# Optimization experiments

Hardware: AMD Instinct MI355X
Metric: run time of the kernel (lower is better)

## Reference

```python
import jax, jax.numpy as jnp
import numpy as np

HEADS = 16
NEG = -10000.0


def setup_inputs() -> dict:
    key = jax.random.key(0)
    ks = jax.random.split(key, 8)
    B, S, D = 2, 2048, 2048
    scale = 0.02
    return {
        "q": jax.random.normal(ks[0], (B, S, D), dtype=jnp.float32),
        "k": jax.random.normal(ks[1], (B, S, D), dtype=jnp.float32),
        "v": jax.random.normal(ks[2], (B, S, D), dtype=jnp.float32),
        "mask": jax.random.randint(ks[3], (B, S, S), 0, 2).astype(jnp.bool_),
        "Wq": jax.random.normal(ks[4], (D, D), dtype=jnp.float32) * scale,
        "Wk": jax.random.normal(ks[5], (D, D), dtype=jnp.float32) * scale,
        "Wv": jax.random.normal(ks[6], (D, D), dtype=jnp.float32) * scale,
        "Wo": jax.random.normal(ks[7], (D, D), dtype=jnp.float32) * scale,
    }


def _split_heads(x):
    # (B, S, D) -> (B, H, S, Dh)
    B, S, D = x.shape
    return x.reshape(B, S, HEADS, D // HEADS).transpose(0, 2, 1, 3)


def reference(q, k, v, mask, Wq, Wk, Wv, Wo):
    # bias-free linear projections (nn.Linear: x @ W.T)
    qp = q @ Wq.T
    kp = k @ Wk.T
    vp = v @ Wv.T
    qh, kh, vh = _split_heads(qp), _split_heads(kp), _split_heads(vp)
    head_dim = qh.shape[-1]
    # scores: (B, H, S, S)
    scores = jnp.einsum('bhqd,bhkd->bhqk', qh, kh) / jnp.sqrt(
        jnp.asarray(head_dim, dtype=qh.dtype))
    # additive mask, broadcast over heads (mask unsqueezed at -3 in torch)
    scores = scores + mask[:, None, :, :].astype(scores.dtype) * NEG
    attn = jax.nn.softmax(scores, axis=-1)
    ctx = jnp.einsum('bhqk,bhkd->bhqd', attn, vh)  # (B, H, S, Dh)
    B, H, S, Dh = ctx.shape
    ctx = ctx.transpose(0, 2, 1, 3).reshape(B, S, H * Dh)
    out = ctx @ Wo.T
    return (out, kp, vp)
```

## Files before the change

### kernel.cpp

```cpp
#include <hip/hip_runtime.h>
#include <hip/hip_bf16.h>
#include <stdint.h>


typedef unsigned short u16;
typedef unsigned char u8;
typedef __bf16 bf16x8 __attribute__((ext_vector_type(8)));
typedef unsigned short u16x8 __attribute__((ext_vector_type(8)));
typedef unsigned short u16x4 __attribute__((ext_vector_type(4)));
typedef float f32x4 __attribute__((ext_vector_type(4)));

#if __has_builtin(__builtin_amdgcn_exp2f)
#define EXP2(x) __builtin_amdgcn_exp2f(x)
#else
#define EXP2(x) exp2f(x)
#endif

__device__ __forceinline__ u16 f2bf(float f) {
  union { __bf16 h; u16 u; } c;
  c.h = (__bf16)f;
  return c.u;
}

__device__ __forceinline__ void stage8_f32(const float* src, u16* dst) {
  float4 x0 = ((const float4*)src)[0];
  float4 x1 = ((const float4*)src)[1];
  u16 t[8] = {f2bf(x0.x), f2bf(x0.y), f2bf(x0.z), f2bf(x0.w),
              f2bf(x1.x), f2bf(x1.y), f2bf(x1.z), f2bf(x1.w)};
  *(uint4*)dst = *(const uint4*)t;
}

typedef const __attribute__((address_space(1))) void gas_t;
typedef __attribute__((address_space(3))) void las_t;
__device__ __forceinline__ void gll16(const void* g, void* l) {
  __builtin_amdgcn_global_load_lds((gas_t*)g, (las_t*)l, 16, 0, 0);
}

__global__ void detect_kernel(const u16* __restrict__ q,
                              const u16* __restrict__ mask,
                              int* __restrict__ flags) {
  __shared__ int c32, oddnz, b3f80;
  if (threadIdx.x == 0) { c32 = 0; oddnz = 0; b3f80 = 0; }
  __syncthreads();
  int l32 = 0, lodd = 0, l3f = 0;
  for (int i = threadIdx.x; i < 4096; i += 256) {
    u16 u = q[i];
    if (((u >> 7) & 0xFF) >= 0x86) l32++;
    u16 m = mask[i];
    if (m == 0x3F80) l3f++;
    if ((i & 1) && m != 0) lodd++;
  }
  if (l32) atomicAdd(&c32, l32);
  if (lodd) atomicAdd(&oddnz, lodd);
  if (l3f) atomicAdd(&b3f80, l3f);
  __syncthreads();
  if (threadIdx.x == 0) {
    flags[0] = (c32 > 16) ? 1 : 0;
    flags[1] = b3f80 ? 2 : (oddnz ? 1 : 0);
  }
}

__global__ void pack_mask(const u8* __restrict__ maskp,
                          const int* __restrict__ flags,
                          u16* __restrict__ bits, long n) {
  const int mm = flags[1];
  long gw = ((long)blockIdx.x * blockDim.x + threadIdx.x) >> 6;
  int lane = threadIdx.x & 63;
  long nw = ((long)gridDim.x * blockDim.x) >> 6;
  for (long w = gw; w * 64 < n; w += nw) {
    long i = w * 64 + lane;
    bool nz;
    if (mm == 0)      nz = ((const int*)maskp)[i] != 0;
    else if (mm == 1) nz = maskp[i] != 0;
    else              nz = ((const u16*)maskp)[i] != 0;
    unsigned long long b = __ballot(nz);
    if (lane < 4) bits[w * 4 + lane] = (u16)(b >> (lane * 16));
  }
}

__global__ __launch_bounds__(256) void to_bf16_all(
    const u8* __restrict__ q, const u8* __restrict__ k, const u8* __restrict__ v,
    const u8* __restrict__ wq, const u8* __restrict__ wk,
    const u8* __restrict__ wv, const u8* __restrict__ wo,
    u16* __restrict__ qi, u16* __restrict__ ki, u16* __restrict__ vi,
    u16* __restrict__ wqb, u16* __restrict__ wkb, u16* __restrict__ wvb,
    u16* __restrict__ wob, const int* __restrict__ flags, long NEa, long NW) {
  const int fp = flags[0];
  const u8* src; u16* dst; long n;
  switch (blockIdx.y) {
    case 0: src = q;  dst = qi;  n = NEa; break;
    case 1: src = k;  dst = ki;  n = NEa; break;
    case 2: src = v;  dst = vi;  n = NEa; break;
    case 3: src = wq; dst = wqb; n = NW;  break;
    case 4: src = wk; dst = wkb; n = NW;  break;
    case 5: src = wv; dst = wvb; n = NW;  break;
    default: src = wo; dst = wob; n = NW; break;
  }
  long i0 = ((long)blockIdx.x * 256 + threadIdx.x) * 8;
  long stride = (long)gridDim.x * 256 * 8;
  for (long i = i0; i < n; i += stride) {
    u16 tmp[8];
    if (fp) stage8_f32((const float*)src + i, tmp);
    else    *(uint4*)tmp = *(const uint4*)((const u16*)src + i);
    *(uint4*)&dst[i] = *(const uint4*)tmp;
  }
}

__global__ __launch_bounds__(256) void transpose_v(
    const u8* __restrict__ vpbase, u16* __restrict__ vt,
    const int* __restrict__ flags, long NE, int B, int S, int H) {
  __shared__ u16 T[128 * 128];
  const int fp = flags[0];
  const int tid = threadIdx.x;
  const int s0 = blockIdx.x * 128, h = blockIdx.y, b = blockIdx.z;
  const int D = H * 128;
#pragma unroll
  for (int i = 0; i < 8; i++) {
    int t2 = i * 256 + tid;
    int si = t2 >> 4, cd = (t2 & 15) * 8;
    long off = (long)(b * S + s0 + si) * D + h * 128 + cd;
    u16 tmp[8];
    if (fp) stage8_f32((const float*)vpbase + 2 * NE + off, tmp);
    else    *(uint4*)tmp = *(const uint4*)((const u16*)vpbase + 2 * NE + off);
#pragma unroll
    for (int e = 0; e < 8; e++) {
      int d = cd + e;
      T[d * 128 + (si ^ (d & 15))] = tmp[e];
    }
  }
  __syncthreads();
#pragma unroll
  for (int i = 0; i < 8; i++) {
    int t2 = i * 256 + tid;
    int d = t2 >> 4, sc = (t2 & 15) * 8;
    u16 tmp[8];
#pragma unroll
    for (int e = 0; e < 8; e++)
      tmp[e] = T[d * 128 + ((sc + e) ^ (d & 15))];
    *(uint4*)&vt[((long)(b * H + h) * 128 + d) * S + s0 + sc] = *(const uint4*)tmp;
  }
}

#define BM 128
#define BN 128
#define BK 32

__device__ __forceinline__ void gemm_stage(
    const u8* __restrict__ Ab, const u8* __restrict__ Wbase,
    u16* __restrict__ AsD, u16* __restrict__ WsD,
    bool abf, bool wbf, int bm, int bn, int K, int k0, int tid, int wave) {
#pragma unroll
  for (int i = 0; i < 2; i++) {
    int t = i * 256 + tid;
    int r = t >> 2, c = (t & 3) * 8;
    long aoff = (long)(bm + r) * K + k0 + c;
    long woff = (long)(bn + r) * K + k0 + c;
    if (abf) gll16((const u16*)Ab + aoff, &AsD[(i * 256 + wave * 64) * 8]);
    else     stage8_f32((const float*)Ab + aoff, &AsD[t * 8]);
    if (wbf) gll16((const u16*)Wbase + woff, &WsD[(i * 256 + wave * 64) * 8]);
    else     stage8_f32((const float*)Wbase + woff, &WsD[t * 8]);
  }
}

__global__ __launch_bounds__(256) void gemm_xwT(
    const u8* __restrict__ Abase, const u8* __restrict__ Abase2,
    const u8* __restrict__ Abase3, const u8* __restrict__ Wbase,
    u8* __restrict__ Cbase, int c_slot, int amode, int qkv,
    const int* __restrict__ flags, int M, int N, int K,
    u16* __restrict__ dualbf) {
  __shared__ __align__(16) u16 As[2][BM * BK];
  __shared__ __align__(16) u16 Ws[2][BN * BK];
  const int fp = flags[0];
  const bool abf = (amode == 2) || (amode == 0) || !fp;
  const bool wbf = (amode == 2) || !fp;
  const int tid = threadIdx.x;
  const int wave = tid >> 6, lane = tid & 63;
  const int lq = lane >> 4, lm = lane & 15;
  const int n = blockIdx.x;
  const int nbx = N >> 7;
  const int t3 = n >> 3;
  const int bx = t3 % nbx;
  const int by = (n & 7) + 8 * (t3 / nbx);
  const int bm = by * BM, bn = bx * BN;
  const int wm = (wave >> 1) * 64, wn = (wave & 1) * 64;
  const long MN = (long)M * N;
  const u8* Ab = Abase;
  if (qkv) {
    int blk = bn >> 11;
    Ab = (blk == 0) ? Abase : (blk == 1) ? Abase2 : Abase3;
  }
  f32x4 acc[4][4] = {};

  gemm_stage(Ab, Wbase, As[0], Ws[0], abf, wbf, bm, bn, K, 0, tid, wave);
  __syncthreads();

  int cur = 0;
  for (int k0 = 0; k0 < K; k0 += BK) {
    if (k0 + BK < K)
      gemm_stage(Ab, Wbase, As[cur ^ 1], Ws[cur ^ 1], abf, wbf,
                 bm, bn, K, k0 + BK, tid, wave);
    bf16x8 af[4], wf[4];
#pragma unroll
    for (int i = 0; i < 4; i++)
      af[i] = *(const bf16x8*)&As[cur][(wm + i * 16 + lm) * BK + lq * 8];
#pragma unroll
    for (int j = 0; j < 4; j++)
      wf[j] = *(const bf16x8*)&Ws[cur][(wn + j * 16 + lm) * BK + lq * 8];
#pragma unroll
    for (int i = 0; i < 4; i++)
#pragma unroll
      for (int j = 0; j < 4; j++)
        acc[i][j] = __builtin_amdgcn_mfma_f32_16x16x32_bf16(af[i], wf[j], acc[i][j], 0, 0, 0);
    __syncthreads();
    cur ^= 1;
  }

  if (qkv) {
    const long NE2 = (long)M * 2048;
    const int blk = bn >> 11;
#pragma unroll
    for (int i = 0; i < 4; i++)
#pragma unroll
      for (int j = 0; j < 4; j++) {
        int col = bn + wn + j * 16 + lm;
        int lc = col & 2047;
#pragma unroll
        for (int r = 0; r < 4; r++) {
          int row = bm + wm + i * 16 + lq * 4 + r;
          long idx = (long)row * 2048 + lc;
          float v = acc[i][j][r];
          if (blk == 0) {
            ((u16*)Cbase)[idx] = f2bf(v);
          } else {
            if (fp) ((float*)Cbase)[(long)blk * NE2 + idx] = v;
            else    ((u16*)Cbase)[(long)blk * NE2 + idx] = f2bf(v);
            if (blk == 1) dualbf[idx] = f2bf(v);
          }
        }
      }
  } else {
#pragma unroll
    for (int i = 0; i < 4; i++)
#pragma unroll
      for (int j = 0; j < 4; j++)
#pragma unroll
        for (int r = 0; r < 4; r++) {
          int row = bm + wm + i * 16 + lq * 4 + r;
          int col = bn + wn + j * 16 + lm;
          long idx = (long)row * N + col;
          float v = acc[i][j][r];
          if (dualbf) dualbf[idx] = f2bf(v);
          if (c_slot < 0)  ((u16*)Cbase)[idx] = f2bf(v);
          else if (fp)     ((float*)Cbase)[(long)c_slot * MN + idx] = v;
          else             ((u16*)Cbase)[(long)c_slot * MN + idx] = f2bf(v);
        }
  }
}

#define AQ 128
#define AK 64
#define DH 128

__device__ __forceinline__ void attn_stage(
    int kb, u16* __restrict__ KsD, u16* __restrict__ VsD,
    const u16* __restrict__ kbf, const u8* __restrict__ kvbase,
    const u16* __restrict__ vtb, int use_kbf, int use_vt, int fp,
    long NE, int b, int h, int S, int D, int tid, int w) {
  const long kvoff = ((long)b * S + kb) * D + h * DH;
#pragma unroll
  for (int i = 0; i < 2; i++) {
    int t = i * 512 + tid;
    int r = t >> 4, c8 = t & 15;
    if (use_kbf) {
      gll16(kbf + kvoff + (long)r * D + (c8 ^ ((r & 3) << 2)) * 8,
            &KsD[(i * 512 + w * 64) * 8]);
    } else if (!fp) {
      gll16((const u16*)kvbase + NE + kvoff + (long)r * D + (c8 ^ ((r & 3) << 2)) * 8,
            &KsD[(i * 512 + w * 64) * 8]);
    } else {
      stage8_f32((const float*)kvbase + NE + kvoff + (long)r * D + (c8 ^ ((r & 3) << 2)) * 8,
                 &KsD[t * 8]);
    }
    if (use_vt) {
      int d = t >> 3, c = t & 7;
      gll16(vtb + (long)d * S + kb + ((c ^ (d & 7)) * 8),
            &VsD[(i * 512 + w * 64) * 8]);
    } else if (!fp) {
      gll16((const u16*)kvbase + 2 * NE + kvoff + (long)r * D + (c8 ^ (((r >> 3) & 3) << 1)) * 8,
            &VsD[(i * 512 + w * 64) * 8]);
    } else {
      stage8_f32((const float*)kvbase + 2 * NE + kvoff + (long)r * D + (c8 ^ (((r >> 3) & 3) << 1)) * 8,
                 &VsD[t * 8]);
    }
  }
}

__global__ __launch_bounds__(512) void attn_kernel(
    const u16* __restrict__ qp, const u8* __restrict__ kvbase,
    const u16* __restrict__ vt, const u16* __restrict__ kbf,
    const u8* __restrict__ maskp, const u16* __restrict__ bits,
    u16* __restrict__ ctx, const int* __restrict__ flags,
    int use_bits, int use_vt, int use_kbf, long NE, int B, int S, int H) {
  __shared__ __align__(16) u16 Ks[2][AK * DH];
  __shared__ __align__(16) u16 Vs[2][AK * DH];
  __shared__ __align__(16) u16 Ps[AQ * AK];
  const int fp = flags[0];
  const int mm = flags[1];
  const int tid = threadIdx.x;
  const int w = tid >> 6, lane = tid & 63;
  const int lq = lane >> 4, lm = lane & 15;
  const int nblk = blockIdx.x;
  const int q0 = ((nblk >> 3) & 15) * AQ;
  const int bh = (nblk >> 7) * 8 + (nblk & 7);
  const int h = bh & 15, b = bh >> 4;
  const int D = H * DH;
  const long qbase = ((long)b * S + q0) * D + h * DH;
  const u16* vtb = vt + (long)(b * H + h) * DH * S;
  const float C1 = 0.12751744f;
  const float CN = -28.8539008f;
  const float CM = -14455.8043f;
  const float CL = 86.5617f;

  bf16x8 qf[4];
#pragma unroll
  for (int ks = 0; ks < 4; ks++)
    qf[ks] = *(const bf16x8*)&qp[qbase + (long)(w * 16 + lm) * D + ks * 32 + lq * 8];

  float lrow[4] = {0.f, 0.f, 0.f, 0.f};
  f32x4 oacc[8] = {};

  attn_stage(0, Ks[0], Vs[0], kbf, kvbase, vtb, use_kbf, use_vt, fp,
             NE, b, h, S, D, tid, w);
  __syncthreads();

  int cur = 0;
  for (int kb = 0; kb < S; kb += AK) {
    u16x4 mbv[4];
    if (use_bits) {
#pragma unroll
      for (int r = 0; r < 4; r++) {
        int row = q0 + w * 16 + lq * 4 + r;
        mbv[r] = *(const u16x4*)&bits[(long)b * S * (S >> 4) + (long)row * (S >> 4) + (kb >> 4)];
      }
    }

    if (kb + AK < S)
      attn_stage(kb + AK, Ks[cur ^ 1], Vs[cur ^ 1], kbf, kvbase, vtb,
                 use_kbf, use_vt, fp, NE, b, h, S, D, tid, w);

    f32x4 sacc[4] = {};
#pragma unroll
    for (int ks = 0; ks < 4; ks++)
#pragma unroll
      for (int j = 0; j < 4; j++) {
        int krow = j * 16 + lm;
        int cc = (ks * 4 + lq) ^ ((lm & 3) << 2);
        bf16x8 kf = *(const bf16x8*)&Ks[cur][krow * DH + cc * 8];
        sacc[j] = __builtin_amdgcn_mfma_f32_16x16x32_bf16(qf[ks], kf, sacc[j], 0, 0, 0);
      }

#pragma unroll
    for (int j = 0; j < 4; j++)
#pragma unroll
      for (int r = 0; r < 4; r++) {
        bool mk;
        if (use_bits) {
          mk = (mbv[r][j] >> lm) & 1;
        } else {
          int row = q0 + w * 16 + lq * 4 + r;
          long midx = (long)b * S * S + (long)row * S + kb + j * 16 + lm;
          if (mm == 0)      mk = ((const int*)maskp)[midx] != 0;
          else if (mm == 1) mk = maskp[midx] != 0;
          else              mk = ((const u16*)maskp)[midx] != 0;
        }
        float arg = fmaf(sacc[j][r], C1, mk ? CM : CN);
        float p = EXP2(fminf(arg, CL));
        lrow[r] += p;
        Ps[(w * 16 + lq * 4 + r) * AK + ((j * 16 + lm) ^ (lq << 4))] = f2bf(p);
      }

#pragma unroll
    for (int ks2 = 0; ks2 < 2; ks2++) {
      int prow = w * 16 + lm;
      int cb = (ks2 * 32 + lq * 8) ^ (((lm >> 2) & 3) << 4);
      bf16x8 pf = *(const bf16x8*)&Ps[prow * AK + cb];
      if (use_vt) {
#pragma unroll
        for (int tn = 0; tn < 8; tn++) {
          int d = tn * 16 + lm;
          int p = (ks2 * 4 + lq) ^ (lm & 7);
          bf16x8 vf = *(const bf16x8*)&Vs[cur][d * 64 + p * 8];
          oacc[tn] = __builtin_amdgcn_mfma_f32_16x16x32_bf16(pf, vf, oacc[tn], 0, 0, 0);
        }
      } else {
#pragma unroll
        for (int tn = 0; tn < 8; tn++) {
          u16x8 vtmp;
#pragma unroll
          for (int jj = 0; jj < 8; jj++) {
            int s = ks2 * 32 + lq * 8 + jj;
            int d = (tn * 16 + lm) ^ (lq << 4);
            vtmp[jj] = Vs[cur][s * DH + d];
          }
          bf16x8 vf = __builtin_bit_cast(bf16x8, vtmp);
          oacc[tn] = __builtin_amdgcn_mfma_f32_16x16x32_bf16(pf, vf, oacc[tn], 0, 0, 0);
        }
      }
    }

    __syncthreads();
    cur ^= 1;
  }

  float linv[4];
#pragma unroll
  for (int r = 0; r < 4; r++) {
    float l = lrow[r];
#pragma unroll
    for (int o = 1; o < 16; o <<= 1) l += __shfl_xor(l, o);
    linv[r] = 1.f / fmaxf(l, 1e-30f);
  }
#pragma unroll
  for (int tn = 0; tn < 8; tn++)
#pragma unroll
    for (int r = 0; r < 4; r++) {
      int row = w * 16 + lq * 4 + r;
      int col = tn * 16 + lm;
      ctx[qbase + (long)row * D + col] = f2bf(oacc[tn][r] * linv[r]);
    }
}

extern "C" void kernel_launch(void* const* d_in, const int* in_sizes, int n_in,
                              void* d_out, int out_size, void* d_ws, size_t ws_size,
                              hipStream_t stream) {
  const int Bb = 2, S = 2048, Dm = 2048, H = 16;
  const int M = Bb * S;
  const long NE = (long)M * Dm;
  const long NEb = NE * 2;
  const long NW = (long)Dm * Dm;
  const long Wb = NW * 2;
  const long bits_bytes = (long)Bb * S * (S / 16) * 2;

  char* ws = (char*)d_ws;
  const size_t o_flags = (size_t)NEb;
  const size_t o_bits  = o_flags + 64;
  const size_t o_vt    = o_bits + (size_t)bits_bytes;
  const size_t o_kbf   = o_vt + (size_t)NEb;
  const size_t o_qi    = o_kbf + (size_t)NEb;
  const size_t o_ki    = o_qi + (size_t)NEb;
  const size_t o_vi    = o_ki + (size_t)NEb;
  const size_t o_wq    = o_vi + (size_t)NEb;
  const size_t o_wk    = o_wq + (size_t)Wb;
  const size_t o_wv    = o_wk + (size_t)Wb;
  const size_t o_wo    = o_wv + (size_t)Wb;
  const size_t o_end   = o_wo + (size_t)Wb;

  u16* qp    = (u16*)d_out;
  u16* ctx   = (u16*)ws;
  int* flags = (int*)(ws + o_flags);
  u16* bits  = (u16*)(ws + o_bits);
  u16* vt    = (u16*)(ws + o_vt);
  u16* kbf   = (u16*)(ws + o_kbf);
  u16* qi    = (u16*)(ws + o_qi);
  u16* ki    = (u16*)(ws + o_ki);
  u16* vi    = (u16*)(ws + o_vi);
  u16* wqb   = (u16*)(ws + o_wq);
  u16* wkb   = (u16*)(ws + o_wk);
  u16* wvb   = (u16*)(ws + o_wv);
  u16* wob   = (u16*)(ws + o_wo);

  const int use_bits = (ws_size >= o_vt)  ? 1 : 0;
  const int use_vt   = (ws_size >= o_kbf) ? 1 : 0;
  const int use_kbf  = (ws_size >= o_qi)  ? 1 : 0;
  const int use_conv = (ws_size >= o_end) ? 1 : 0;

  detect_kernel<<<1, 256, 0, stream>>>((const u16*)d_in[0], (const u16*)d_in[3], flags);
  if (use_bits)
    pack_mask<<<1024, 256, 0, stream>>>((const u8*)d_in[3], flags, bits, (long)Bb * S * S);

  dim3 gg(512);
  if (use_conv) {
    to_bf16_all<<<dim3(1024, 7), 256, 0, stream>>>(
        (const u8*)d_in[0], (const u8*)d_in[1], (const u8*)d_in[2],
        (const u8*)d_in[4], (const u8*)d_in[5], (const u8*)d_in[6], (const u8*)d_in[7],
        qi, ki, vi, wqb, wkb, wvb, wob, flags, NE, NW);
    gemm_xwT<<<dim3((M / 128) * (3 * Dm / 128)), 256, 0, stream>>>(
        (const u8*)qi, (const u8*)ki, (const u8*)vi, (const u8*)wqb,
        (u8*)d_out, 0, 2, 1, flags, M, 3 * Dm, Dm, kbf);
  } else {
    gemm_xwT<<<gg, 256, 0, stream>>>((const u8*)d_in[0], nullptr, nullptr,
                                     (const u8*)d_in[4],
                                     (u8*)qp, -1, 1, 0, flags, M, Dm, Dm, nullptr);
    gemm_xwT<<<gg, 256, 0, stream>>>((const u8*)d_in[1], nullptr, nullptr,
                                     (const u8*)d_in[5],
                                     (u8*)d_out, 1, 1, 0, flags, M, Dm, Dm,
                                     use_kbf ? kbf : nullptr);
    gemm_xwT<<<gg, 256, 0, stream>>>((const u8*)d_in[2], nullptr, nullptr,
                                     (const u8*)d_in[6],
                                     (u8*)d_out, 2, 1, 0, flags, M, Dm, Dm, nullptr);
  }
  if (use_vt)
    transpose_v<<<dim3(S / 128, H, Bb), 256, 0, stream>>>(
        (const u8*)d_out, vt, flags, NE, Bb, S, H);
  attn_kernel<<<dim3(512), 512, 0, stream>>>(
      qp, (const u8*)d_out, vt, kbf, (const u8*)d_in[3], bits, ctx, flags,
      use_bits, use_vt, use_kbf, NE, Bb, S, H);
  gemm_xwT<<<gg, 256, 0, stream>>>((const u8*)ctx, nullptr, nullptr,
                                   use_conv ? (const u8*)wob : (const u8*)d_in[7],
                                   (u8*)d_out, 0, use_conv ? 2 : 0, 0, flags, M, Dm, Dm, nullptr);
}
```

Measured before the change: 631.1 us.

## Triple-buffer GEMM loads with vmcnt waits; single-buffer V in attention

```diff
diff --git a/kernel.cpp b/kernel.cpp
--- a/kernel.cpp
+++ b/kernel.cpp
@@ -168,11 +168,12 @@
     u8* __restrict__ Cbase, int c_slot, int amode, int qkv,
     const int* __restrict__ flags, int M, int N, int K,
     u16* __restrict__ dualbf) {
-  __shared__ __align__(16) u16 As[2][BM * BK];
-  __shared__ __align__(16) u16 Ws[2][BN * BK];
+  __shared__ __align__(16) u16 As[3][BM * BK];
+  __shared__ __align__(16) u16 Ws[3][BN * BK];
   const int fp = flags[0];
   const bool abf = (amode == 2) || (amode == 0) || !fp;
   const bool wbf = (amode == 2) || !fp;
+  const bool pure = abf && wbf;
   const int tid = threadIdx.x;
   const int wave = tid >> 6, lane = tid & 63;
   const int lq = lane >> 4, lm = lane & 15;
@@ -192,13 +193,25 @@
   f32x4 acc[4][4] = {};
 
   gemm_stage(Ab, Wbase, As[0], Ws[0], abf, wbf, bm, bn, K, 0, tid, wave);
-  __syncthreads();
+  if (BK < K)
+    gemm_stage(Ab, Wbase, As[1], Ws[1], abf, wbf, bm, bn, K, BK, tid, wave);
 
   int cur = 0;
   for (int k0 = 0; k0 < K; k0 += BK) {
-    if (k0 + BK < K)
-      gemm_stage(Ab, Wbase, As[cur ^ 1], Ws[cur ^ 1], abf, wbf,
-                 bm, bn, K, k0 + BK, tid, wave);
+    const bool more1 = (k0 + BK < K);
+    const bool more2 = (k0 + 2 * BK < K);
+    if (pure) {
+      if (more1) asm volatile("s_waitcnt vmcnt(4)" ::: "memory");
+      else       asm volatile("s_waitcnt vmcnt(0)" ::: "memory");
+      __builtin_amdgcn_s_barrier();
+    } else {
+      __syncthreads();
+    }
+    if (more2) {
+      int nxt = cur + 2; if (nxt >= 3) nxt -= 3;
+      gemm_stage(Ab, Wbase, As[nxt], Ws[nxt], abf, wbf,
+                 bm, bn, K, k0 + 2 * BK, tid, wave);
+    }
     bf16x8 af[4], wf[4];
 #pragma unroll
     for (int i = 0; i < 4; i++)
@@ -211,8 +224,7 @@
 #pragma unroll
       for (int j = 0; j < 4; j++)
         acc[i][j] = __builtin_amdgcn_mfma_f32_16x16x32_bf16(af[i], wf[j], acc[i][j], 0, 0, 0);
-    __syncthreads();
-    cur ^= 1;
+    cur += 1; if (cur >= 3) cur -= 3;
   }
 
   if (qkv) {
@@ -261,11 +273,10 @@
 #define AK 64
 #define DH 128
 
-__device__ __forceinline__ void attn_stage(
-    int kb, u16* __restrict__ KsD, u16* __restrict__ VsD,
+__device__ __forceinline__ void attn_stageK(
+    int kb, u16* __restrict__ KsD,
     const u16* __restrict__ kbf, const u8* __restrict__ kvbase,
-    const u16* __restrict__ vtb, int use_kbf, int use_vt, int fp,
-    long NE, int b, int h, int S, int D, int tid, int w) {
+    int use_kbf, int fp, long NE, int b, int h, int S, int D, int tid, int w) {
   const long kvoff = ((long)b * S + kb) * D + h * DH;
 #pragma unroll
   for (int i = 0; i < 2; i++) {
@@ -281,6 +292,18 @@
       stage8_f32((const float*)kvbase + NE + kvoff + (long)r * D + (c8 ^ ((r & 3) << 2)) * 8,
                  &KsD[t * 8]);
     }
+  }
+}
+
+__device__ __forceinline__ void attn_stageV(
+    int kb, u16* __restrict__ VsD,
+    const u8* __restrict__ kvbase, const u16* __restrict__ vtb,
+    int use_vt, int fp, long NE, int b, int h, int S, int D, int tid, int w) {
+  const long kvoff = ((long)b * S + kb) * D + h * DH;
+#pragma unroll
+  for (int i = 0; i < 2; i++) {
+    int t = i * 512 + tid;
+    int r = t >> 4, c8 = t & 15;
     if (use_vt) {
       int d = t >> 3, c = t & 7;
       gll16(vtb + (long)d * S + kb + ((c ^ (d & 7)) * 8),
@@ -302,7 +325,7 @@
     u16* __restrict__ ctx, const int* __restrict__ flags,
     int use_bits, int use_vt, int use_kbf, long NE, int B, int S, int H) {
   __shared__ __align__(16) u16 Ks[2][AK * DH];
-  __shared__ __align__(16) u16 Vs[2][AK * DH];
+  __shared__ __align__(16) u16 Vs[AK * DH];
   __shared__ __align__(16) u16 Ps[AQ * AK];
   const int fp = flags[0];
   const int mm = flags[1];
@@ -329,12 +352,13 @@
   float lrow[4] = {0.f, 0.f, 0.f, 0.f};
   f32x4 oacc[8] = {};
 
-  attn_stage(0, Ks[0], Vs[0], kbf, kvbase, vtb, use_kbf, use_vt, fp,
-             NE, b, h, S, D, tid, w);
+  attn_stageK(0, Ks[0], kbf, kvbase, use_kbf, fp, NE, b, h, S, D, tid, w);
+  attn_stageV(0, Vs, kvbase, vtb, use_vt, fp, NE, b, h, S, D, tid, w);
   __syncthreads();
 
   int cur = 0;
   for (int kb = 0; kb < S; kb += AK) {
+    const bool more = (kb + AK < S);
     u16x4 mbv[4];
     if (use_bits) {
 #pragma unroll
@@ -344,9 +368,9 @@
       }
     }
 
-    if (kb + AK < S)
-      attn_stage(kb + AK, Ks[cur ^ 1], Vs[cur ^ 1], kbf, kvbase, vtb,
-                 use_kbf, use_vt, fp, NE, b, h, S, D, tid, w);
+    if (more)
+      attn_stageK(kb + AK, Ks[cur ^ 1], kbf, kvbase, use_kbf, fp,
+                  NE, b, h, S, D, tid, w);
 
     f32x4 sacc[4] = {};
 #pragma unroll
@@ -379,6 +403,8 @@
         Ps[(w * 16 + lq * 4 + r) * AK + ((j * 16 + lm) ^ (lq << 4))] = f2bf(p);
       }
 
+    __syncthreads();
+
 #pragma unroll
     for (int ks2 = 0; ks2 < 2; ks2++) {
       int prow = w * 16 + lm;
@@ -389,7 +415,7 @@
         for (int tn = 0; tn < 8; tn++) {
           int d = tn * 16 + lm;
           int p = (ks2 * 4 + lq) ^ (lm & 7);
-          bf16x8 vf = *(const bf16x8*)&Vs[cur][d * 64 + p * 8];
+          bf16x8 vf = *(const bf16x8*)&Vs[d * 64 + p * 8];
           oacc[tn] = __builtin_amdgcn_mfma_f32_16x16x32_bf16(pf, vf, oacc[tn], 0, 0, 0);
         }
       } else {
@@ -400,7 +426,7 @@
           for (int jj = 0; jj < 8; jj++) {
             int s = ks2 * 32 + lq * 8 + jj;
             int d = (tn * 16 + lm) ^ (lq << 4);
-            vtmp[jj] = Vs[cur][s * DH + d];
+            vtmp[jj] = Vs[s * DH + d];
           }
           bf16x8 vf = __builtin_bit_cast(bf16x8, vtmp);
           oacc[tn] = __builtin_amdgcn_mfma_f32_16x16x32_bf16(pf, vf, oacc[tn], 0, 0, 0);
@@ -409,6 +435,9 @@
     }
 
     __syncthreads();
+    if (more)
+      attn_stageV(kb + AK, Vs, kvbase, vtb, use_vt, fp,
+                  NE, b, h, S, D, tid, w);
     cur ^= 1;
   }
 
```

After: 632.1 us. Within noise of the previous version (+0.1%).
